# Optimization experiments

Measured on AMD Instinct MI355X. Metric: run time of the kernel, lower is better.

## Reference

```python
import jax, jax.numpy as jnp
import numpy as np

NUM_ITERATIONS = 3
SOFTMAX_DIM = 1  # softmax over out_capsules


def _squash(x, axis=-1):
    # scale = ||x|| / (1 + ||x||^2)  (leftthomas/CapsuleLayer squash)
    norm = jnp.linalg.norm(x, axis=axis, keepdims=True)
    return x * (norm / (1.0 + norm * norm))


def _normalize(x, axis=-1, eps=1e-12):
    n = jnp.linalg.norm(x, axis=axis, keepdims=True)
    return x / jnp.maximum(n, eps)


def setup_inputs() -> dict:
    key = jax.random.key(0)
    k1, k2, k3 = jax.random.split(key, 3)
    B, I, O, LIN, LOUT = 64, 512, 64, 8, 16
    x = jax.random.normal(k1, (B, I, LIN), dtype=jnp.float32)
    # xavier-uniform over last two dims of the 4D weight
    limit = float(np.sqrt(6.0 / (LIN + LOUT)))
    weight = jax.random.uniform(k2, (O, I, LOUT, LIN), jnp.float32, -limit, limit)
    blim = float(np.sqrt(6.0 / (O + LOUT)))
    bias = jax.random.uniform(k3, (O, LOUT), jnp.float32, -blim, blim)
    return {"x": x, "weight": weight, "bias": bias}


def reference(x, weight, bias):
    # priors[b,o,i,v] = sum_l weight[o,i,v,l] * x[b,i,l]  -> [B, O, I, Lout]
    priors = jnp.einsum('oivl,bil->boiv', weight, x)
    # k-means routing, 'dot' similarity
    out = jnp.mean(priors, axis=-2, keepdims=True)  # [B, O, 1, Lout]
    for _ in range(NUM_ITERATIONS):
        logits = jnp.sum(priors * _normalize(out, axis=-1), axis=-1, keepdims=True)  # [B,O,I,1]
        probs = jax.nn.softmax(logits, axis=SOFTMAX_DIM)  # over out_capsules
        out = jnp.sum(probs * priors, axis=-2, keepdims=True)  # [B,O,1,Lout]
    out = _squash(out, axis=-1).squeeze(-2)  # [B, O, Lout]
    return out + bias
```

## Files before the change

### kernel.cpp

```cpp
#include <hip/hip_runtime.h>
#include <hip/hip_bf16.h>
#include <cstdint>


typedef float float4v __attribute__((ext_vector_type(4)));
typedef unsigned short ushort8 __attribute__((ext_vector_type(8)));

__device__ __forceinline__ float bf2f(unsigned short u) {
    union { unsigned int ui; float f; } cv;
    cv.ui = ((unsigned int)u) << 16;
    return cv.f;
}
__device__ __forceinline__ unsigned short f2bf(float f) {
    union { float f; unsigned int ui; } cv;
    cv.f = f;
    unsigned int u = cv.ui;
    unsigned int r = u + 0x7FFFu + ((u >> 16) & 1u);
    return (unsigned short)(r >> 16);
}

__global__ __launch_bounds__(256) void k_priors(const float* __restrict__ W,
                                                const float* __restrict__ x,
                                                unsigned short* __restrict__ priors) {
    const int i = blockIdx.x;
    const int t = threadIdx.x;
    __shared__ float Wl[16 * 132];
    __shared__ float xl[512];

    if (t < 128) {
        float4v v = *(const float4v*)(x + ((size_t)(t >> 1) * 512 + i) * 8 + (size_t)(t & 1) * 4);
        *(float4v*)(xl + t * 4) = v;
    }

    const int r  = t & 15;
    const int bq = t >> 4;

    for (int oc = 0; oc < 4; ++oc) {
        __syncthreads();
        #pragma unroll
        for (int k = 0; k < 2; ++k) {
            int j  = t + k * 256;
            int ol = j >> 5;
            int r4 = j & 31;
            float4v v = *(const float4v*)(W + ((size_t)((oc * 16 + ol) * 512 + i)) * 128 + (size_t)r4 * 4);
            *(float4v*)(Wl + ol * 132 + r4 * 4) = v;
        }
        __syncthreads();

        float4v wreg[32];
        const float4v* wp = (const float4v*)(Wl + r * 132);
        #pragma unroll
        for (int j = 0; j < 32; ++j) wreg[j] = wp[j];

        const int o = oc * 16 + r;
        #pragma unroll
        for (int k = 0; k < 4; ++k) {
            const int b = bq + 16 * k;
            float4v xr0 = ((const float4v*)(xl + b * 8))[0];
            float4v xr1 = ((const float4v*)(xl + b * 8))[1];
            ushort8 u0, u1;
            #pragma unroll
            for (int v = 0; v < 16; ++v) {
                float s = 0.0f;
                #pragma unroll
                for (int l = 0; l < 8; ++l) {
                    int idx = v * 8 + l;
                    float wv = wreg[idx >> 2][idx & 3];
                    float xv = (l < 4) ? xr0[l & 3] : xr1[l & 3];
                    s = fmaf(wv, xv, s);
                }
                unsigned short hb = f2bf(s);
                if (v < 8) u0[v] = hb; else u1[v - 8] = hb;
            }
            unsigned short* dst = priors + ((size_t)(b * 512 + i) * 64 + o) * 16;
            *(ushort8*)(dst) = u0;
            *(ushort8*)(dst + 8) = u1;
        }
    }
}

__global__ __launch_bounds__(256) void k_sum0(const unsigned short* __restrict__ priors,
                                              float* __restrict__ part0) {
    const int b    = blockIdx.x >> 4;
    const int ic   = blockIdx.x & 15;
    const int t    = threadIdx.x;
    const int slot = t & 127;
    const int io   = t >> 7;
    const int o    = slot >> 1;
    const int vh   = slot & 1;

    float acc[8];
    #pragma unroll
    for (int j = 0; j < 8; ++j) acc[j] = 0.0f;

    const unsigned short* base = priors + (size_t)b * 524288 + (size_t)o * 16 + vh * 8;
    #pragma unroll
    for (int k = 0; k < 16; ++k) {
        const int i = ic * 32 + k * 2 + io;
        ushort8 u = *(const ushort8*)(base + (size_t)i * 1024);
        #pragma unroll
        for (int j = 0; j < 8; ++j) acc[j] += bf2f(u[j]);
    }

    __shared__ float red[8 * 128];
    if (io == 1) {
        #pragma unroll
        for (int j = 0; j < 8; ++j) red[j * 128 + slot] = acc[j];
    }
    __syncthreads();
    if (io == 0) {
        float* dst = part0 + (size_t)b * 16384 + (size_t)ic * 1024 + o * 16 + vh * 8;
        #pragma unroll
        for (int j = 0; j < 8; ++j) dst[j] = acc[j] + red[j * 128 + slot];
    }
}

__global__ __launch_bounds__(256) void k_route(const unsigned short* __restrict__ priors,
                                               const float* __restrict__ part_prev,
                                               float* __restrict__ part_next) {
    const int b    = blockIdx.x >> 4;
    const int h    = blockIdx.x & 15;
    const int t    = threadIdx.x;
    const int w    = t >> 6;
    const int lane = t & 63;

    __shared__ float noutT[16 * 64];
    __shared__ float accbuf[4 * 1088];

    if (t < 64) {
        const float* pp = part_prev + (size_t)b * 16384 + t * 16;
        float4v s4[4];
        #pragma unroll
        for (int g = 0; g < 4; ++g) s4[g] = (float4v){0.f, 0.f, 0.f, 0.f};
        #pragma unroll
        for (int ic = 0; ic < 16; ++ic) {
            #pragma unroll
            for (int g = 0; g < 4; ++g)
                s4[g] += *(const float4v*)(pp + (size_t)ic * 1024 + g * 4);
        }
        float vv[16]; float n2 = 0.0f;
        #pragma unroll
        for (int j = 0; j < 16; ++j) { vv[j] = s4[j >> 2][j & 3]; n2 += vv[j] * vv[j]; }
        float inv = 1.0f / fmaxf(sqrtf(n2), 1e-12f);
        #pragma unroll
        for (int j = 0; j < 16; ++j) noutT[j * 64 + t] = vv[j] * inv;
    }
    __syncthreads();

    float nr[16];
    #pragma unroll
    for (int j = 0; j < 16; ++j) nr[j] = noutT[j * 64 + lane];

    float acc[16];
    #pragma unroll
    for (int j = 0; j < 16; ++j) acc[j] = 0.0f;

    const size_t base = (size_t)b * 524288 + (size_t)lane * 16;
    #pragma unroll
    for (int k = 0; k < 8; ++k) {
        const int i = h * 32 + w + 4 * k;
        const ushort8* pp = (const ushort8*)(priors + base + (size_t)i * 1024);
        ushort8 u0 = pp[0], u1 = pp[1];
        float pf[16];
        #pragma unroll
        for (int j = 0; j < 8; ++j) { pf[j] = bf2f(u0[j]); pf[8 + j] = bf2f(u1[j]); }

        float logit = 0.0f;
        #pragma unroll
        for (int j = 0; j < 16; ++j) logit = fmaf(pf[j], nr[j], logit);

        float m = logit;
        #pragma unroll
        for (int d = 1; d < 64; d <<= 1) m = fmaxf(m, __shfl_xor(m, d));
        float e = __expf(logit - m);
        float s = e;
        #pragma unroll
        for (int d = 1; d < 64; d <<= 1) s += __shfl_xor(s, d);
        float p = e / s;

        #pragma unroll
        for (int j = 0; j < 16; ++j) acc[j] = fmaf(p, pf[j], acc[j]);
    }

    #pragma unroll
    for (int j = 0; j < 16; ++j) accbuf[w * 1088 + lane * 17 + j] = acc[j];
    __syncthreads();

    float* dst = part_next + (size_t)b * 16384 + (size_t)h * 1024;
    for (int j = t; j < 1024; j += 256) {
        const int o = j >> 4, v = j & 15;
        const int idx = o * 17 + v;
        dst[j] = accbuf[idx] + accbuf[1088 + idx] + accbuf[2176 + idx] + accbuf[3264 + idx];
    }
}

__global__ __launch_bounds__(64) void k_fin(const float* __restrict__ part3,
                                            const float* __restrict__ bias,
                                            float* __restrict__ out) {
    const int b = blockIdx.x;
    const int o = threadIdx.x;
    const float* pp = part3 + (size_t)b * 16384 + o * 16;
    float4v s4[4];
    #pragma unroll
    for (int g = 0; g < 4; ++g) s4[g] = (float4v){0.f, 0.f, 0.f, 0.f};
    #pragma unroll
    for (int ic = 0; ic < 16; ++ic) {
        #pragma unroll
        for (int g = 0; g < 4; ++g)
            s4[g] += *(const float4v*)(pp + (size_t)ic * 1024 + g * 4);
    }
    float vv[16]; float n2 = 0.0f;
    #pragma unroll
    for (int j = 0; j < 16; ++j) { vv[j] = s4[j >> 2][j & 3]; n2 += vv[j] * vv[j]; }
    float n = sqrtf(n2);
    float scale = n / (1.0f + n2);
    float* q = out + (size_t)b * 1024 + o * 16;
    #pragma unroll
    for (int j = 0; j < 16; ++j) q[j] = vv[j] * scale + bias[o * 16 + j];
}

extern "C" void kernel_launch(void* const* d_in, const int* in_sizes, int n_in,
                              void* d_out, int out_size, void* d_ws, size_t ws_size,
                              hipStream_t stream) {
    const float* x    = (const float*)d_in[0];
    const float* W    = (const float*)d_in[1];
    const float* bias = (const float*)d_in[2];
    float* out = (float*)d_out;

    unsigned short* priors = (unsigned short*)d_ws;
    float* part = (float*)((char*)d_ws + (size_t)64 * 512 * 64 * 16 * 2);
    float* part0 = part;
    float* part1 = part + 1048576;
    float* part2 = part + 2 * 1048576;
    float* part3 = part + 3 * 1048576;

    k_priors<<<512, 256, 0, stream>>>(W, x, priors);
    k_sum0  <<<1024, 256, 0, stream>>>(priors, part0);
    k_route <<<1024, 256, 0, stream>>>(priors, part0, part1);
    k_route <<<1024, 256, 0, stream>>>(priors, part1, part2);
    k_route <<<1024, 256, 0, stream>>>(priors, part2, part3);
    k_fin   <<<64, 64, 0, stream>>>(part3, bias, out);
}
```

Before: 106.0 us.

## Fuse prior computation with initial sum and fold finalize into last route

Merges the priors kernel with the initial mean reduction: threads now accumulate each computed prior directly into per-chunk partial sums instead of re-reading the bf16 priors buffer. The priors kernel is reorganized over (batch-group, i-chunk) blocks with W read straight from global memory. The final squash and bias step is folded into the last routing kernel using a per-batch atomic counter, so the last block to finish a batch does the finalize. This saves one kernel launch and one pass over the priors. In exchange it adds a memset, atomics and fences, and reduces the priors grid to 256 blocks.

After: 189.2 us. 1.78x slower.

```diff
diff --git a/kernel.cpp b/kernel.cpp
--- a/kernel.cpp
+++ b/kernel.cpp
@@ -5,6 +5,7 @@
 
 typedef float float4v __attribute__((ext_vector_type(4)));
 typedef unsigned short ushort8 __attribute__((ext_vector_type(8)));
+typedef unsigned short ushort4v __attribute__((ext_vector_type(4)));
 
 __device__ __forceinline__ float bf2f(unsigned short u) {
     union { unsigned int ui; float f; } cv;
@@ -19,99 +20,65 @@
     return (unsigned short)(r >> 16);
 }
 
-__global__ __launch_bounds__(256) void k_priors(const float* __restrict__ W,
-                                                const float* __restrict__ x,
-                                                unsigned short* __restrict__ priors) {
-    const int i = blockIdx.x;
-    const int t = threadIdx.x;
-    __shared__ float Wl[16 * 132];
-    __shared__ float xl[512];
-
-    if (t < 128) {
-        float4v v = *(const float4v*)(x + ((size_t)(t >> 1) * 512 + i) * 8 + (size_t)(t & 1) * 4);
-        *(float4v*)(xl + t * 4) = v;
-    }
-
-    const int r  = t & 15;
-    const int bq = t >> 4;
-
-    for (int oc = 0; oc < 4; ++oc) {
-        __syncthreads();
-        #pragma unroll
-        for (int k = 0; k < 2; ++k) {
-            int j  = t + k * 256;
-            int ol = j >> 5;
-            int r4 = j & 31;
-            float4v v = *(const float4v*)(W + ((size_t)((oc * 16 + ol) * 512 + i)) * 128 + (size_t)r4 * 4);
-            *(float4v*)(Wl + ol * 132 + r4 * 4) = v;
-        }
-        __syncthreads();
-
-        float4v wreg[32];
-        const float4v* wp = (const float4v*)(Wl + r * 132);
-        #pragma unroll
-        for (int j = 0; j < 32; ++j) wreg[j] = wp[j];
-
-        const int o = oc * 16 + r;
-        #pragma unroll
-        for (int k = 0; k < 4; ++k) {
-            const int b = bq + 16 * k;
-            float4v xr0 = ((const float4v*)(xl + b * 8))[0];
-            float4v xr1 = ((const float4v*)(xl + b * 8))[1];
-            ushort8 u0, u1;
-            #pragma unroll
-            for (int v = 0; v < 16; ++v) {
+__global__ __launch_bounds__(256) void k_pri_sum(const float* __restrict__ W,
+                                                 const float* __restrict__ x,
+                                                 unsigned short* __restrict__ priors,
+                                                 float* __restrict__ part0) {
+    const int ic = blockIdx.x & 15;
+    const int bg = blockIdx.x >> 4;
+    const int t  = threadIdx.x;
+    const int o  = t >> 2;
+    const int vh = t & 3;
+
+    __shared__ float xl[4][32][8];
+    {
+        const int bl  = t >> 6;
+        const int il  = (t & 63) >> 1;
+        const int hf  = t & 1;
+        const float* src = x + ((size_t)((bg * 4 + bl) * 512 + ic * 32 + il)) * 8 + hf * 4;
+        *(float4v*)(&xl[bl][il][hf * 4]) = *(const float4v*)src;
+    }
+    __syncthreads();
+
+    float4v acc[4];
+    #pragma unroll
+    for (int j = 0; j < 4; ++j) acc[j] = (float4v){0.f, 0.f, 0.f, 0.f};
+
+    const float* wbase = W + (size_t)o * 65536 + (size_t)(ic * 32) * 128 + vh * 32;
+
+    for (int il = 0; il < 32; ++il) {
+        float4v wq[8];
+        #pragma unroll
+        for (int j = 0; j < 8; ++j) wq[j] = *(const float4v*)(wbase + (size_t)il * 128 + j * 4);
+        const int i = ic * 32 + il;
+        #pragma unroll
+        for (int bl = 0; bl < 4; ++bl) {
+            float4v xr0 = *(const float4v*)(&xl[bl][il][0]);
+            float4v xr1 = *(const float4v*)(&xl[bl][il][4]);
+            ushort4v u;
+            #pragma unroll
+            for (int v = 0; v < 4; ++v) {
                 float s = 0.0f;
                 #pragma unroll
                 for (int l = 0; l < 8; ++l) {
-                    int idx = v * 8 + l;
-                    float wv = wreg[idx >> 2][idx & 3];
+                    float wv = wq[v * 2 + (l >> 2)][l & 3];
                     float xv = (l < 4) ? xr0[l & 3] : xr1[l & 3];
                     s = fmaf(wv, xv, s);
                 }
-                unsigned short hb = f2bf(s);
-                if (v < 8) u0[v] = hb; else u1[v - 8] = hb;
+                acc[bl][v] += s;
+                u[v] = f2bf(s);
             }
-            unsigned short* dst = priors + ((size_t)(b * 512 + i) * 64 + o) * 16;
-            *(ushort8*)(dst) = u0;
-            *(ushort8*)(dst + 8) = u1;
-        }
-    }
-}
-
-__global__ __launch_bounds__(256) void k_sum0(const unsigned short* __restrict__ priors,
-                                              float* __restrict__ part0) {
-    const int b    = blockIdx.x >> 4;
-    const int ic   = blockIdx.x & 15;
-    const int t    = threadIdx.x;
-    const int slot = t & 127;
-    const int io   = t >> 7;
-    const int o    = slot >> 1;
-    const int vh   = slot & 1;
-
-    float acc[8];
-    #pragma unroll
-    for (int j = 0; j < 8; ++j) acc[j] = 0.0f;
-
-    const unsigned short* base = priors + (size_t)b * 524288 + (size_t)o * 16 + vh * 8;
-    #pragma unroll
-    for (int k = 0; k < 16; ++k) {
-        const int i = ic * 32 + k * 2 + io;
-        ushort8 u = *(const ushort8*)(base + (size_t)i * 1024);
-        #pragma unroll
-        for (int j = 0; j < 8; ++j) acc[j] += bf2f(u[j]);
-    }
-
-    __shared__ float red[8 * 128];
-    if (io == 1) {
-        #pragma unroll
-        for (int j = 0; j < 8; ++j) red[j * 128 + slot] = acc[j];
-    }
-    __syncthreads();
-    if (io == 0) {
-        float* dst = part0 + (size_t)b * 16384 + (size_t)ic * 1024 + o * 16 + vh * 8;
-        #pragma unroll
-        for (int j = 0; j < 8; ++j) dst[j] = acc[j] + red[j * 128 + slot];
+            unsigned short* dst = priors
+                + ((size_t)((bg * 4 + bl) * 512 + i) * 64 + o) * 16 + vh * 4;
+            *(ushort4v*)dst = u;
+        }
+    }
+
+    #pragma unroll
+    for (int bl = 0; bl < 4; ++bl) {
+        float* dst = part0 + (size_t)(bg * 4 + bl) * 16384 + (size_t)ic * 1024
+                   + o * 16 + vh * 4;
+        *(float4v*)dst = acc[bl];
     }
 }
 
@@ -194,29 +161,114 @@
     }
 }
 
-__global__ __launch_bounds__(64) void k_fin(const float* __restrict__ part3,
-                                            const float* __restrict__ bias,
-                                            float* __restrict__ out) {
-    const int b = blockIdx.x;
-    const int o = threadIdx.x;
-    const float* pp = part3 + (size_t)b * 16384 + o * 16;
-    float4v s4[4];
-    #pragma unroll
-    for (int g = 0; g < 4; ++g) s4[g] = (float4v){0.f, 0.f, 0.f, 0.f};
-    #pragma unroll
-    for (int ic = 0; ic < 16; ++ic) {
-        #pragma unroll
-        for (int g = 0; g < 4; ++g)
-            s4[g] += *(const float4v*)(pp + (size_t)ic * 1024 + g * 4);
-    }
-    float vv[16]; float n2 = 0.0f;
-    #pragma unroll
-    for (int j = 0; j < 16; ++j) { vv[j] = s4[j >> 2][j & 3]; n2 += vv[j] * vv[j]; }
-    float n = sqrtf(n2);
-    float scale = n / (1.0f + n2);
-    float* q = out + (size_t)b * 1024 + o * 16;
-    #pragma unroll
-    for (int j = 0; j < 16; ++j) q[j] = vv[j] * scale + bias[o * 16 + j];
+__global__ __launch_bounds__(256) void k_route_fin(const unsigned short* __restrict__ priors,
+                                                   const float* __restrict__ part_prev,
+                                                   float* __restrict__ part_next,
+                                                   const float* __restrict__ bias,
+                                                   float* __restrict__ out,
+                                                   int* __restrict__ bcnt) {
+    const int b    = blockIdx.x >> 4;
+    const int h    = blockIdx.x & 15;
+    const int t    = threadIdx.x;
+    const int w    = t >> 6;
+    const int lane = t & 63;
+
+    __shared__ float noutT[16 * 64];
+    __shared__ float accbuf[4 * 1088];
+    __shared__ int islast;
+
+    if (t < 64) {
+        const float* pp = part_prev + (size_t)b * 16384 + t * 16;
+        float4v s4[4];
+        #pragma unroll
+        for (int g = 0; g < 4; ++g) s4[g] = (float4v){0.f, 0.f, 0.f, 0.f};
+        #pragma unroll
+        for (int ic = 0; ic < 16; ++ic) {
+            #pragma unroll
+            for (int g = 0; g < 4; ++g)
+                s4[g] += *(const float4v*)(pp + (size_t)ic * 1024 + g * 4);
+        }
+        float vv[16]; float n2 = 0.0f;
+        #pragma unroll
+        for (int j = 0; j < 16; ++j) { vv[j] = s4[j >> 2][j & 3]; n2 += vv[j] * vv[j]; }
+        float inv = 1.0f / fmaxf(sqrtf(n2), 1e-12f);
+        #pragma unroll
+        for (int j = 0; j < 16; ++j) noutT[j * 64 + t] = vv[j] * inv;
+    }
+    __syncthreads();
+
+    float nr[16];
+    #pragma unroll
+    for (int j = 0; j < 16; ++j) nr[j] = noutT[j * 64 + lane];
+
+    float acc[16];
+    #pragma unroll
+    for (int j = 0; j < 16; ++j) acc[j] = 0.0f;
+
+    const size_t base = (size_t)b * 524288 + (size_t)lane * 16;
+    #pragma unroll
+    for (int k = 0; k < 8; ++k) {
+        const int i = h * 32 + w + 4 * k;
+        const ushort8* pp = (const ushort8*)(priors + base + (size_t)i * 1024);
+        ushort8 u0 = pp[0], u1 = pp[1];
+        float pf[16];
+        #pragma unroll
+        for (int j = 0; j < 8; ++j) { pf[j] = bf2f(u0[j]); pf[8 + j] = bf2f(u1[j]); }
+
+        float logit = 0.0f;
+        #pragma unroll
+        for (int j = 0; j < 16; ++j) logit = fmaf(pf[j], nr[j], logit);
+
+        float m = logit;
+        #pragma unroll
+        for (int d = 1; d < 64; d <<= 1) m = fmaxf(m, __shfl_xor(m, d));
+        float e = __expf(logit - m);
+        float s = e;
+        #pragma unroll
+        for (int d = 1; d < 64; d <<= 1) s += __shfl_xor(s, d);
+        float p = e / s;
+
+        #pragma unroll
+        for (int j = 0; j < 16; ++j) acc[j] = fmaf(p, pf[j], acc[j]);
+    }
+
+    #pragma unroll
+    for (int j = 0; j < 16; ++j) accbuf[w * 1088 + lane * 17 + j] = acc[j];
+    __syncthreads();
+
+    float* dst = part_next + (size_t)b * 16384 + (size_t)h * 1024;
+    for (int j = t; j < 1024; j += 256) {
+        const int o = j >> 4, v = j & 15;
+        const int idx = o * 17 + v;
+        dst[j] = accbuf[idx] + accbuf[1088 + idx] + accbuf[2176 + idx] + accbuf[3264 + idx];
+    }
+
+    __syncthreads();
+    if (t == 0) {
+        __threadfence();
+        int old = __hip_atomic_fetch_add(&bcnt[b], 1, __ATOMIC_ACQ_REL,
+                                         __HIP_MEMORY_SCOPE_AGENT);
+        islast = (old == 15) ? 1 : 0;
+    }
+    __syncthreads();
+    if (islast && t < 64) {
+        const float* p3 = part_next + (size_t)b * 16384 + t * 16;
+        float vv[16]; float n2 = 0.0f;
+        #pragma unroll
+        for (int j = 0; j < 16; ++j) {
+            float s = 0.0f;
+            #pragma unroll
+            for (int ic = 0; ic < 16; ++ic)
+                s += __hip_atomic_load(p3 + (size_t)ic * 1024 + j,
+                                       __ATOMIC_RELAXED, __HIP_MEMORY_SCOPE_AGENT);
+            vv[j] = s; n2 += s * s;
+        }
+        float n = sqrtf(n2);
+        float sc = n / (1.0f + n2);
+        float* qd = out + (size_t)b * 1024 + t * 16;
+        #pragma unroll
+        for (int j = 0; j < 16; ++j) qd[j] = vv[j] * sc + bias[t * 16 + j];
+    }
 }
 
 extern "C" void kernel_launch(void* const* d_in, const int* in_sizes, int n_in,
@@ -228,16 +280,15 @@
     float* out = (float*)d_out;
 
     unsigned short* priors = (unsigned short*)d_ws;
-    float* part = (float*)((char*)d_ws + (size_t)64 * 512 * 64 * 16 * 2);
-    float* part0 = part;
-    float* part1 = part + 1048576;
-    float* part2 = part + 2 * 1048576;
-    float* part3 = part + 3 * 1048576;
-
-    k_priors<<<512, 256, 0, stream>>>(W, x, priors);
-    k_sum0  <<<1024, 256, 0, stream>>>(priors, part0);
-    k_route <<<1024, 256, 0, stream>>>(priors, part0, part1);
-    k_route <<<1024, 256, 0, stream>>>(priors, part1, part2);
-    k_route <<<1024, 256, 0, stream>>>(priors, part2, part3);
-    k_fin   <<<64, 64, 0, stream>>>(part3, bias, out);
-}
+    float* p0 = (float*)((char*)d_ws + 67108864);
+    float* p1 = (float*)((char*)d_ws + 71303168);
+    float* p2 = (float*)((char*)d_ws + 75497472);
+    int* bcnt = (int*)((char*)d_ws + 79691776);
+    float* p3 = p0;
+
+    hipMemsetAsync(bcnt, 0, 256, stream);
+    k_pri_sum  <<<256,  256, 0, stream>>>(W, x, priors, p0);
+    k_route    <<<1024, 256, 0, stream>>>(priors, p0, p1);
+    k_route    <<<1024, 256, 0, stream>>>(priors, p1, p2);
+    k_route_fin<<<1024, 256, 0, stream>>>(priors, p2, p3, bias, out, bcnt);
+}
```
